# Performance work log

Measured on AMD Instinct MI355X. Metric: run time of the kernel, lower is better.

Reference implementation:

```python
import jax, jax.numpy as jnp
import numpy as np

N_NODES = 50000
N_EDGES = 800000
N_GRAPHS = 256
IN_DIM = 128
HID = 64
HEADS = 4
N_CLASSES = 2
NEG_SLOPE = 0.2


def gat_conv(h, W, attn_l, attn_r, bias, src, dst, n_heads, out_dim):
    """DGL-style GATConv. h: [N, Fin] -> [N, H, D]."""
    n = h.shape[0]
    feat = (h @ W).reshape(n, n_heads, out_dim)            # [N,H,D]
    el = jnp.sum(feat * attn_l, axis=-1)                   # [N,H]
    er = jnp.sum(feat * attn_r, axis=-1)                   # [N,H]
    e = jax.nn.leaky_relu(el[src] + er[dst], NEG_SLOPE)    # [E,H]
    # edge softmax over incoming edges of each dst node (numerically stable)
    emax = jax.ops.segment_max(e, dst, num_segments=n)     # [N,H]
    emax = jnp.where(jnp.isfinite(emax), emax, 0.0)
    ee = jnp.exp(e - emax[dst])                            # [E,H]
    denom = jax.ops.segment_sum(ee, dst, num_segments=n)   # [N,H]
    alpha = ee / jnp.maximum(denom, 1e-9)[dst]             # [E,H]
    msg = alpha[:, :, None] * feat[src]                    # [E,H,D]
    rst = jax.ops.segment_sum(msg, dst, num_segments=n)    # [N,H,D]
    return rst + bias.reshape(1, n_heads, out_dim)


def setup_inputs() -> dict:
    key = jax.random.key(0)
    ks = jax.random.split(key, 16)
    h = jax.random.normal(ks[0], (N_NODES, IN_DIM), dtype=jnp.float32)
    src = jax.random.randint(ks[1], (N_EDGES,), 0, N_NODES, dtype=jnp.int32)
    dst = jax.random.randint(ks[2], (N_EDGES,), 0, N_NODES, dtype=jnp.int32)
    graph_ids = jnp.sort(jax.random.randint(ks[3], (N_NODES,), 0, N_GRAPHS, dtype=jnp.int32))
    s1 = 1.0 / np.sqrt(IN_DIM)
    s2 = 1.0 / np.sqrt(HID * HEADS)
    sc = 1.0 / np.sqrt(HID)
    W1 = jax.random.normal(ks[4], (IN_DIM, HEADS * HID), dtype=jnp.float32) * s1
    attn_l1 = jax.random.normal(ks[5], (HEADS, HID), dtype=jnp.float32) * sc
    attn_r1 = jax.random.normal(ks[6], (HEADS, HID), dtype=jnp.float32) * sc
    b1 = jnp.zeros((HEADS * HID,), dtype=jnp.float32)
    W2 = jax.random.normal(ks[7], (HEADS * HID, 1 * HID), dtype=jnp.float32) * s2
    attn_l2 = jax.random.normal(ks[8], (1, HID), dtype=jnp.float32) * sc
    attn_r2 = jax.random.normal(ks[9], (1, HID), dtype=jnp.float32) * sc
    b2 = jnp.zeros((HID,), dtype=jnp.float32)
    Wc = jax.random.normal(ks[10], (HID, N_CLASSES), dtype=jnp.float32) * sc
    bc = jnp.zeros((N_CLASSES,), dtype=jnp.float32)
    return {"h": h, "src": src, "dst": dst, "graph_ids": graph_ids,
            "W1": W1, "attn_l1": attn_l1, "attn_r1": attn_r1, "b1": b1,
            "W2": W2, "attn_l2": attn_l2, "attn_r2": attn_r2, "b2": b2,
            "Wc": Wc, "bc": bc}


def reference(h, src, dst, graph_ids, W1, attn_l1, attn_r1, b1,
              W2, attn_l2, attn_r2, b2, Wc, bc):
    # layer 1: [N, IN] -> [N, HEADS, HID] -> relu -> flatten heads
    x = jax.nn.relu(gat_conv(h, W1, attn_l1, attn_r1, b1, src, dst, HEADS, HID))
    x = x.reshape(N_NODES, HEADS * HID)
    # layer 2: single head -> [N, HID]
    x = jax.nn.relu(gat_conv(x, W2, attn_l2, attn_r2, b2, src, dst, 1, HID))
    x = x.reshape(N_NODES, HID)
    # dropout p=0.3 is identity at eval time
    # AvgPooling: mean of node features per graph
    sums = jax.ops.segment_sum(x, graph_ids, num_segments=N_GRAPHS)      # [G,HID]
    cnts = jax.ops.segment_sum(jnp.ones((N_NODES,), x.dtype), graph_ids,
                               num_segments=N_GRAPHS)                    # [G]
    pooled = sums / jnp.maximum(cnts, 1.0)[:, None]
    return pooled @ Wc + bc                                              # [G, n_classes]
```

## Files before the change

kernel.cpp:

```cpp
#include <hip/hip_runtime.h>
#include <math.h>

#define NN 50000
#define NE 800000
#define NG 256
#define IND 128
#define NBUCK 98
#define CHUNK 4096
#define NPBLK ((NE + CHUNK - 1) / CHUNK)

typedef __bf16 bf16_t;
typedef bf16_t bf16x8 __attribute__((ext_vector_type(8)));
typedef float f32x4 __attribute__((ext_vector_type(4)));
typedef float floatx2 __attribute__((ext_vector_type(2)));
typedef unsigned short ushortx8 __attribute__((ext_vector_type(8)));

__device__ __forceinline__ float lrelu(float x) { return fmaxf(x, 0.2f * x); }
__device__ __forceinline__ float b2f(unsigned short u) {
  return __uint_as_float(((unsigned)u) << 16);
}
__device__ __forceinline__ unsigned short f2b(float f) {
  unsigned u = __float_as_uint(f);
  return (unsigned short)((u + 0x7fffu + ((u >> 16) & 1u)) >> 16);
}
__device__ __forceinline__ float sel4(float v0, float v1, float v2, float v3, int g) {
  float a01 = (g & 1) ? v1 : v0;
  float a23 = (g & 1) ? v3 : v2;
  return (g & 2) ? a23 : a01;
}

__global__ __launch_bounds__(256) void k_prep(const float* __restrict__ W1,
                                              const int* __restrict__ dst,
                                              unsigned short* __restrict__ w1t_hi,
                                              int* __restrict__ counts) {
  int tid = blockIdx.x * 256 + threadIdx.x;
  if (tid < 256 * IND) {
    int c = tid >> 7, k = tid & 127;
    w1t_hi[tid] = f2b(W1[(size_t)k * 256 + c]);
  }
  if (tid < NE) atomicAdd(&counts[dst[tid]], 1);
}

__global__ __launch_bounds__(256) void k_gemm1(const float* __restrict__ h,
                                               const unsigned short* __restrict__ w1t_hi,
                                               const float* __restrict__ al,
                                               const float* __restrict__ ar,
                                               unsigned int* __restrict__ feat1f8,
                                               float4* __restrict__ el1,
                                               float4* __restrict__ er1) {
  __shared__ unsigned short w1s[256 * IND];
  int t = threadIdx.x;
  for (int i = t; i < 4096; i += 256) {
    int c = i >> 4, k8 = i & 15;
    ushortx8 v = ((const ushortx8*)w1t_hi)[i];
    int byte = (c * 256 + k8 * 16) ^ ((c & 7) << 4);
    *(ushortx8*)((char*)w1s + byte) = v;
  }
  __syncthreads();
  int w = t >> 6, l = t & 63;
  int c0 = l & 15, kg = l >> 4;
  int rw = blockIdx.x * 64 + w * 16;
  int arow = rw + c0;
  if (arow >= NN) arow = NN - 1;
  const float4* hp = (const float4*)h + (size_t)arow * 32 + kg * 2;
  f32x4 acc[16] = {};
#pragma unroll
  for (int ks = 0; ks < 4; ks++) {
    float4 v0 = hp[ks * 8], v1 = hp[ks * 8 + 1];
    float f[8] = {v0.x, v0.y, v0.z, v0.w, v1.x, v1.y, v1.z, v1.w};
    ushortx8 uh, ul;
#pragma unroll
    for (int j = 0; j < 8; j++) {
      unsigned short hj = f2b(f[j]);
      uh[j] = hj;
      ul[j] = f2b(f[j] - b2f(hj));
    }
    bf16x8 ah = *(bf16x8*)&uh;
    bf16x8 alo = *(bf16x8*)&ul;
#pragma unroll
    for (int n = 0; n < 16; n++) {
      int col = n * 16 + c0;
      int byte = (col * 256 + (ks * 4 + kg) * 16) ^ ((col & 7) << 4);
      bf16x8 b = *(const bf16x8*)(const void*)((const char*)w1s + byte);
      acc[n] = __builtin_amdgcn_mfma_f32_16x16x32_bf16(alo, b, acc[n], 0, 0, 0);
      acc[n] = __builtin_amdgcn_mfma_f32_16x16x32_bf16(ah, b, acc[n], 0, 0, 0);
    }
  }
  float alv[16], arv[16];
#pragma unroll
  for (int n = 0; n < 16; n++) {
    int ai = (n >> 2) * 64 + (n & 3) * 16 + c0;
    alv[n] = al[ai];
    arv[n] = ar[ai];
  }
#pragma unroll
  for (int j = 0; j < 4; j++) {
    int node = rw + kg * 4 + j;
    bool ok = node < NN;
    float pl[4] = {0.f, 0.f, 0.f, 0.f}, pr[4] = {0.f, 0.f, 0.f, 0.f};
#pragma unroll
    for (int dq = 0; dq < 4; dq++) {
      float v0 = acc[dq][j], v1 = acc[4 | dq][j], v2 = acc[8 | dq][j], v3 = acc[12 | dq][j];
      if (ok) {
        int u = __builtin_amdgcn_cvt_pk_fp8_f32(v0, v1, 0, false);
        u = __builtin_amdgcn_cvt_pk_fp8_f32(v2, v3, u, true);
        feat1f8[(size_t)node * 64 + dq * 16 + c0] = (unsigned)u;
      }
    }
#pragma unroll
    for (int n = 0; n < 16; n++) {
      float cv = acc[n][j];
      int hh = n >> 2;
      pl[hh] += cv * alv[n];
      pr[hh] += cv * arv[n];
    }
#pragma unroll
    for (int off = 1; off < 16; off <<= 1) {
#pragma unroll
      for (int hh = 0; hh < 4; hh++) {
        pl[hh] += __shfl_xor(pl[hh], off);
        pr[hh] += __shfl_xor(pr[hh], off);
      }
    }
    if (c0 == 0 && ok) {
      el1[node] = make_float4(pl[0], pl[1], pl[2], pl[3]);
      er1[node] = make_float4(pr[0], pr[1], pr[2], pr[3]);
    }
  }
}

#define NSB ((NN + 1023) / 1024)
__global__ __launch_bounds__(1024) void k_scanA(const int* __restrict__ counts,
                                                int* __restrict__ bsums) {
  int gid = blockIdx.x * 1024 + threadIdx.x;
  int v = (gid < NN) ? counts[gid] : 0;
#pragma unroll
  for (int off = 32; off; off >>= 1) v += __shfl_xor(v, off);
  __shared__ int ws[16];
  int w = threadIdx.x >> 6, l = threadIdx.x & 63;
  if (l == 0) ws[w] = v;
  __syncthreads();
  if (threadIdx.x == 0) {
    int s = 0;
#pragma unroll
    for (int i = 0; i < 16; i++) s += ws[i];
    bsums[blockIdx.x] = s;
  }
}

__global__ __launch_bounds__(64) void k_scanB(const int* __restrict__ bsums,
                                              int* __restrict__ boffs,
                                              int* __restrict__ bcursor) {
  int l = threadIdx.x;
  int orig = (l < NSB) ? bsums[l] : 0;
  int v = orig;
#pragma unroll
  for (int off = 1; off < 64; off <<= 1) {
    int tv = __shfl_up(v, off);
    if (l >= off) v += tv;
  }
  if (l < NSB) boffs[l] = v - orig;
  for (int i = l; i < NBUCK; i += 64) bcursor[i] = 0;
}

__global__ __launch_bounds__(1024) void k_scanC(const int* __restrict__ counts,
                                                const int* __restrict__ boffs,
                                                int* __restrict__ offs) {
  int gid = blockIdx.x * 1024 + threadIdx.x;
  int orig = (gid < NN) ? counts[gid] : 0;
  int v = orig;
  int w = threadIdx.x >> 6, l = threadIdx.x & 63;
#pragma unroll
  for (int off = 1; off < 64; off <<= 1) {
    int tv = __shfl_up(v, off);
    if (l >= off) v += tv;
  }
  __shared__ int ws[16];
  if (l == 63) ws[w] = v;
  __syncthreads();
  int woff = 0;
#pragma unroll
  for (int i = 0; i < 16; i++)
    if (i < w) woff += ws[i];
  if (gid < NN) offs[gid] = boffs[blockIdx.x] + woff + v - orig;
  if (gid == 0) offs[NN] = NE;
}

__global__ __launch_bounds__(256) void k_part(const int* __restrict__ src, const int* __restrict__ dst,
                                              const int* __restrict__ offs, int* __restrict__ bcursor,
                                              int2* __restrict__ ebuf) {
  __shared__ int lcnt[NBUCK];
  __shared__ int lbase[NBUCK];
  __shared__ int gb[NBUCK];
  int t = threadIdx.x;
  for (int i = t; i < NBUCK; i += 256) lcnt[i] = 0;
  __syncthreads();
  int e0 = blockIdx.x * CHUNK;
  int sv[16], dv[16], rk[16];
#pragma unroll
  for (int i = 0; i < 16; i++) {
    int e = e0 + i * 256 + t;
    if (e < NE) {
      sv[i] = src[e];
      dv[i] = dst[e];
      rk[i] = atomicAdd(&lcnt[dv[i] >> 9], 1);
    }
  }
  __syncthreads();
  for (int i = t; i < NBUCK; i += 256) {
    lbase[i] = atomicAdd(&bcursor[i], lcnt[i]);
    gb[i] = offs[i << 9];
  }
  __syncthreads();
#pragma unroll
  for (int i = 0; i < 16; i++) {
    int e = e0 + i * 256 + t;
    if (e < NE) {
      int b = dv[i] >> 9;
      int2 v;
      v.x = sv[i];
      v.y = dv[i];
      ebuf[gb[b] + lbase[b] + rk[i]] = v;
    }
  }
}

__global__ __launch_bounds__(256) void k_scat2(const int2* __restrict__ ebuf, const int* __restrict__ offs,
                                               int2* __restrict__ sd) {
  __shared__ int lcur[512];
  int b = blockIdx.x, t = threadIdx.x;
  for (int i = t; i < 512; i += 256) lcur[i] = 0;
  int n0 = b << 9;
  int n1 = n0 + 512;
  if (n1 > NN) n1 = NN;
  int lo = offs[n0], hi = offs[n1];
  __syncthreads();
  for (int i = lo + t; i < hi; i += 256) {
    int2 p = ebuf[i];
    int pos = atomicAdd(&lcur[p.y - n0], 1);
    sd[offs[p.y] + pos] = p;
  }
}

__global__ __launch_bounds__(256) void k_edge1(const int2* __restrict__ sd,
                                               const float4* __restrict__ el1,
                                               const float4* __restrict__ er1,
                                               ushort4* __restrict__ ee1) {
  int i = blockIdx.x * 256 + threadIdx.x;
  if (i >= NE) return;
  int2 p = sd[i];
  float4 l = el1[p.x], r = er1[p.y];
  ushort4 o;
  o.x = f2b(__expf(lrelu(l.x + r.x)));
  o.y = f2b(__expf(lrelu(l.y + r.y)));
  o.z = f2b(__expf(lrelu(l.z + r.z)));
  o.w = f2b(__expf(lrelu(l.w + r.w)));
  ee1[i] = o;
}

__global__ __launch_bounds__(256) void k_agg1(const int* __restrict__ offs, const int2* __restrict__ sd,
                                              const ushort4* __restrict__ ee1,
                                              const unsigned int* __restrict__ feat1f8,
                                              const float* __restrict__ b1,
                                              unsigned short* __restrict__ x1b) {
  int wid = (blockIdx.x * 256 + threadIdx.x) >> 6;
  int lane = threadIdx.x & 63;
  if (wid >= NN) return;
  int g = lane >> 4, q = lane & 15;
  int start = offs[wid], end = offs[wid + 1];
  float a[4][4] = {};
  float ds0 = 0.f, ds1 = 0.f, ds2 = 0.f, ds3 = 0.f;
  for (int i = start; i < end; i += 4) {
    int e = i + g;
    bool valid = e < end;
    int ec = valid ? e : end - 1;
    int s = sd[ec].x;
    ushort4 wq = ee1[ec];
    float4 wv;
    wv.x = b2f(wq.x); wv.y = b2f(wq.y); wv.z = b2f(wq.z); wv.w = b2f(wq.w);
    if (!valid) { wv.x = 0.f; wv.y = 0.f; wv.z = 0.f; wv.w = 0.f; }
    uint4 u = *(const uint4*)(feat1f8 + (size_t)s * 64 + q * 4);
#pragma unroll
    for (int dj = 0; dj < 4; dj++) {
      unsigned uu = (&u.x)[dj];
      floatx2 lo = __builtin_amdgcn_cvt_pk_f32_fp8(uu, false);
      floatx2 hi = __builtin_amdgcn_cvt_pk_f32_fp8(uu, true);
      a[dj][0] += wv.x * lo[0];
      a[dj][1] += wv.y * lo[1];
      a[dj][2] += wv.z * hi[0];
      a[dj][3] += wv.w * hi[1];
    }
    ds0 += wv.x; ds1 += wv.y; ds2 += wv.z; ds3 += wv.w;
  }
#pragma unroll
  for (int off = 16; off < 64; off <<= 1) {
#pragma unroll
    for (int dj = 0; dj < 4; dj++) {
#pragma unroll
      for (int hh = 0; hh < 4; hh++) a[dj][hh] += __shfl_xor(a[dj][hh], off);
    }
    ds0 += __shfl_xor(ds0, off);
    ds1 += __shfl_xor(ds1, off);
    ds2 += __shfl_xor(ds2, off);
    ds3 += __shfl_xor(ds3, off);
  }
  float dsg = sel4(ds0, ds1, ds2, ds3, g);
  float inv = 1.f / fmaxf(dsg, 1e-9f);
  float4 bb = *(const float4*)(b1 + g * 64 + q * 4);
  ushort4 ov;
  ov.x = f2b(fmaxf(sel4(a[0][0], a[0][1], a[0][2], a[0][3], g) * inv + bb.x, 0.f));
  ov.y = f2b(fmaxf(sel4(a[1][0], a[1][1], a[1][2], a[1][3], g) * inv + bb.y, 0.f));
  ov.z = f2b(fmaxf(sel4(a[2][0], a[2][1], a[2][2], a[2][3], g) * inv + bb.z, 0.f));
  ov.w = f2b(fmaxf(sel4(a[3][0], a[3][1], a[3][2], a[3][3], g) * inv + bb.w, 0.f));
  *(ushort4*)(x1b + (size_t)wid * 256 + g * 64 + q * 4) = ov;
}

__global__ __launch_bounds__(256) void k_gemm2(const unsigned short* __restrict__ x1b,
                                               const float* __restrict__ W2,
                                               const float* __restrict__ al2,
                                               const float* __restrict__ ar2,
                                               unsigned int* __restrict__ feat2f8,
                                               float* __restrict__ el2,
                                               float* __restrict__ er2) {
  __shared__ unsigned short w2t[64 * 256];
  int t = threadIdx.x;
  for (int i = t; i < 64 * 256; i += 256) {
    int k = i >> 6, col = i & 63;
    int kg = k >> 3;
    int s = (col * 32 + kg) ^ (col & 7);
    w2t[s * 8 + (k & 7)] = f2b(W2[i]);
  }
  __syncthreads();
  int w = t >> 6, l = t & 63;
  int rw = blockIdx.x * 64 + w * 16;
  int arow = rw + (l & 15);
  if (arow >= NN) arow = NN - 1;
  const unsigned short* aptr = x1b + (size_t)arow * 256 + (l >> 4) * 8;
  f32x4 acc[4] = {};
#pragma unroll
  for (int ks = 0; ks < 8; ks++) {
    bf16x8 a = *(const bf16x8*)(const void*)(aptr + ks * 32);
#pragma unroll
    for (int n = 0; n < 4; n++) {
      int colg = n * 16 + (l & 15);
      int kg = ks * 4 + (l >> 4);
      int s = (colg * 32 + kg) ^ (colg & 7);
      bf16x8 b = *(const bf16x8*)(const void*)&w2t[s * 8];
      acc[n] = __builtin_amdgcn_mfma_f32_16x16x32_bf16(a, b, acc[n], 0, 0, 0);
    }
  }
  float al2v[4], ar2v[4];
#pragma unroll
  for (int n = 0; n < 4; n++) { al2v[n] = al2[n * 16 + (l & 15)]; ar2v[n] = ar2[n * 16 + (l & 15)]; }
#pragma unroll
  for (int j = 0; j < 4; j++) {
    int node = rw + (l >> 4) * 4 + j;
    float pl = 0.f, pr = 0.f;
    float c0v = acc[0][j], c1v = acc[1][j], c2v = acc[2][j], c3v = acc[3][j];
    if (node < NN) {
      int u = __builtin_amdgcn_cvt_pk_fp8_f32(c0v, c1v, 0, false);
      u = __builtin_amdgcn_cvt_pk_fp8_f32(c2v, c3v, u, true);
      feat2f8[(size_t)node * 16 + (l & 15)] = (unsigned)u;
    }
    pl = c0v * al2v[0] + c1v * al2v[1] + c2v * al2v[2] + c3v * al2v[3];
    pr = c0v * ar2v[0] + c1v * ar2v[1] + c2v * ar2v[2] + c3v * ar2v[3];
#pragma unroll
    for (int off = 1; off < 16; off <<= 1) {
      pl += __shfl_xor(pl, off);
      pr += __shfl_xor(pr, off);
    }
    if ((l & 15) == 0 && node < NN) { el2[node] = pl; er2[node] = pr; }
  }
}

__global__ __launch_bounds__(256) void k_edge2(const int2* __restrict__ sd,
                                               const float* __restrict__ el2,
                                               const float* __restrict__ er2,
                                               float* __restrict__ ee2) {
  int i = blockIdx.x * 256 + threadIdx.x;
  if (i >= NE) return;
  int2 p = sd[i];
  ee2[i] = __expf(lrelu(el2[p.x] + er2[p.y]));
}

__global__ __launch_bounds__(256) void k_agg2(const int* __restrict__ offs, const int2* __restrict__ sd,
                                              const float* __restrict__ ee2,
                                              const unsigned int* __restrict__ feat2f8,
                                              const float* __restrict__ b2, const int* __restrict__ gid,
                                              float* __restrict__ psum) {
  int wid = (blockIdx.x * 256 + threadIdx.x) >> 6;
  int lane = threadIdx.x & 63;
  if (wid >= NN) return;
  int g = lane >> 4, q = lane & 15;
  int start = offs[wid], end = offs[wid + 1];
  float a0 = 0.f, a1 = 0.f, a2 = 0.f, a3 = 0.f, dsum = 0.f;
  for (int i = start; i < end; i += 4) {
    int e = i + g;
    bool valid = e < end;
    int ec = valid ? e : end - 1;
    int s = sd[ec].x;
    float wv = valid ? ee2[ec] : 0.f;
    unsigned u = feat2f8[(size_t)s * 16 + q];
    floatx2 lo = __builtin_amdgcn_cvt_pk_f32_fp8(u, false);
    floatx2 hi = __builtin_amdgcn_cvt_pk_f32_fp8(u, true);
    a0 += wv * lo[0];
    a1 += wv * lo[1];
    a2 += wv * hi[0];
    a3 += wv * hi[1];
    dsum += wv;
  }
#pragma unroll
  for (int off = 16; off < 64; off <<= 1) {
    a0 += __shfl_xor(a0, off);
    a1 += __shfl_xor(a1, off);
    a2 += __shfl_xor(a2, off);
    a3 += __shfl_xor(a3, off);
    dsum += __shfl_xor(dsum, off);
  }
  float inv = 1.f / fmaxf(dsum, 1e-9f);
  float av = sel4(a0, a1, a2, a3, g);
  float v = fmaxf(av * inv + b2[lane], 0.f);
  atomicAdd(&psum[gid[wid] * 64 + lane], v);
}

__global__ __launch_bounds__(256) void k_head(const float* __restrict__ psum, const int* __restrict__ gid,
                                              const float* __restrict__ Wc, const float* __restrict__ bc,
                                              float* __restrict__ out) {
  int wid = (blockIdx.x * 256 + threadIdx.x) >> 6;
  int lane = threadIdx.x & 63;
  if (wid >= NG) return;
  int g = wid;
  int lo = 0, hi = NN;
  while (lo < hi) { int mid = (lo + hi) >> 1; if (gid[mid] < g) lo = mid + 1; else hi = mid; }
  int lb = lo;
  hi = NN;
  while (lo < hi) { int mid = (lo + hi) >> 1; if (gid[mid] < g + 1) lo = mid + 1; else hi = mid; }
  int cnt = lo - lb;
  float inv = 1.f / fmaxf((float)cnt, 1.f);
  float p = psum[g * 64 + lane] * inv;
  float a0 = p * Wc[lane * 2 + 0];
  float a1 = p * Wc[lane * 2 + 1];
#pragma unroll
  for (int off = 32; off; off >>= 1) { a0 += __shfl_xor(a0, off); a1 += __shfl_xor(a1, off); }
  if (lane == 0) { out[g * 2 + 0] = a0 + bc[0]; out[g * 2 + 1] = a1 + bc[1]; }
}

extern "C" void kernel_launch(void* const* d_in, const int* in_sizes, int n_in,
                              void* d_out, int out_size, void* d_ws, size_t ws_size,
                              hipStream_t stream) {
  const float* h = (const float*)d_in[0];
  const int* src = (const int*)d_in[1];
  const int* dst = (const int*)d_in[2];
  const int* gid = (const int*)d_in[3];
  const float* W1 = (const float*)d_in[4];
  const float* al1 = (const float*)d_in[5];
  const float* ar1 = (const float*)d_in[6];
  const float* b1 = (const float*)d_in[7];
  const float* W2 = (const float*)d_in[8];
  const float* al2 = (const float*)d_in[9];
  const float* ar2 = (const float*)d_in[10];
  const float* b2 = (const float*)d_in[11];
  const float* Wc = (const float*)d_in[12];
  const float* bc = (const float*)d_in[13];
  float* out = (float*)d_out;

  char* wsp = (char*)d_ws;
  size_t off = 0;
  auto take = [&](size_t bytes) -> void* {
    void* p = wsp + off;
    off = (off + bytes + 255) & ~(size_t)255;
    return p;
  };
  unsigned int* feat1f8 = (unsigned int*)take((size_t)NN * 256);
  unsigned short* x1b = (unsigned short*)take((size_t)NN * 256 * 2);
  unsigned int* feat2f8 = (unsigned int*)take((size_t)NN * 64);
  unsigned short* w1t_hi = (unsigned short*)take((size_t)256 * IND * 2);
  float4* el1 = (float4*)take((size_t)NN * 16);
  float4* er1 = (float4*)take((size_t)NN * 16);
  float* el2 = (float*)take((size_t)NN * 4);
  float* er2 = (float*)take((size_t)NN * 4);
  int* counts = (int*)take((size_t)NN * 4);
  int* offs = (int*)take((size_t)(NN + 1) * 4);
  int2* sd = (int2*)take((size_t)NE * 8);
  int2* ebuf = (int2*)take((size_t)NE * 8);
  ushort4* ee1 = (ushort4*)take((size_t)NE * 8);
  float* ee2 = (float*)take((size_t)NE * 4);
  float* psum = (float*)take((size_t)NG * 64 * 4);
  int* bsums = (int*)take((size_t)NSB * 4);
  int* boffs = (int*)take((size_t)NSB * 4);
  int* bcursor = (int*)take((size_t)NBUCK * 4);

  hipMemsetAsync(counts, 0, (size_t)NN * 4, stream);
  hipMemsetAsync(psum, 0, (size_t)NG * 64 * 4, stream);

  k_prep<<<(NE + 255) / 256, 256, 0, stream>>>(W1, dst, w1t_hi, counts);

  k_scanA<<<NSB, 1024, 0, stream>>>(counts, bsums);
  k_scanB<<<1, 64, 0, stream>>>(bsums, boffs, bcursor);
  k_scanC<<<NSB, 1024, 0, stream>>>(counts, boffs, offs);
  k_part<<<NPBLK, 256, 0, stream>>>(src, dst, offs, bcursor, ebuf);
  k_scat2<<<NBUCK, 256, 0, stream>>>(ebuf, offs, sd);

  k_gemm1<<<(NN + 63) / 64, 256, 0, stream>>>(h, w1t_hi, al1, ar1, feat1f8, el1, er1);
  k_edge1<<<(NE + 255) / 256, 256, 0, stream>>>(sd, el1, er1, ee1);
  k_agg1<<<(NN * 64 + 255) / 256, 256, 0, stream>>>(offs, sd, ee1, feat1f8, b1, x1b);

  k_gemm2<<<(NN + 63) / 64, 256, 0, stream>>>(x1b, W2, al2, ar2, feat2f8, el2, er2);
  k_edge2<<<(NE + 255) / 256, 256, 0, stream>>>(sd, el2, er2, ee2);
  k_agg2<<<(NN * 64 + 255) / 256, 256, 0, stream>>>(offs, sd, ee2, feat2f8, b2, gid, psum);

  k_head<<<(NG * 64 + 255) / 256, 256, 0, stream>>>(psum, gid, Wc, bc, out);
}
```

Before: 226.8 us.

## Replace atomic graph pooling with bf16 node buffer and per-graph reduction kernel

Layer-2 aggregation now writes per-node outputs as bf16 to a workspace buffer instead of atomically adding into per-graph sums. A new pooling kernel, one 1024-thread block per graph, binary-searches the graph's node range, sums rows in 16 slices through shared memory, then applies the classifier. This removes heavy atomic contention (3.2M atomics onto 16K addresses) and the psum memset, at the cost of an extra 6.4MB write/read round trip and bf16 rounding of layer-2 outputs.

```diff
diff --git a/kernel.cpp b/kernel.cpp
--- a/kernel.cpp
+++ b/kernel.cpp
@@ -386,8 +386,8 @@
 __global__ __launch_bounds__(256) void k_agg2(const int* __restrict__ offs, const int2* __restrict__ sd,
                                               const float* __restrict__ ee2,
                                               const unsigned int* __restrict__ feat2f8,
-                                              const float* __restrict__ b2, const int* __restrict__ gid,
-                                              float* __restrict__ psum) {
+                                              const float* __restrict__ b2,
+                                              unsigned short* __restrict__ x2b) {
   int wid = (blockIdx.x * 256 + threadIdx.x) >> 6;
   int lane = threadIdx.x & 63;
   if (wid >= NN) return;
@@ -419,30 +419,39 @@
   }
   float inv = 1.f / fmaxf(dsum, 1e-9f);
   float av = sel4(a0, a1, a2, a3, g);
-  float v = fmaxf(av * inv + b2[lane], 0.f);
-  atomicAdd(&psum[gid[wid] * 64 + lane], v);
-}
-
-__global__ __launch_bounds__(256) void k_head(const float* __restrict__ psum, const int* __restrict__ gid,
-                                              const float* __restrict__ Wc, const float* __restrict__ bc,
-                                              float* __restrict__ out) {
-  int wid = (blockIdx.x * 256 + threadIdx.x) >> 6;
-  int lane = threadIdx.x & 63;
-  if (wid >= NG) return;
-  int g = wid;
+  x2b[(size_t)wid * 64 + lane] = f2b(fmaxf(av * inv + b2[lane], 0.f));
+}
+
+__global__ __launch_bounds__(1024) void k_pool(const unsigned short* __restrict__ x2b,
+                                               const int* __restrict__ gid,
+                                               const float* __restrict__ Wc,
+                                               const float* __restrict__ bc,
+                                               float* __restrict__ out) {
+  int g = blockIdx.x;
+  int t = threadIdx.x;
   int lo = 0, hi = NN;
   while (lo < hi) { int mid = (lo + hi) >> 1; if (gid[mid] < g) lo = mid + 1; else hi = mid; }
   int lb = lo;
   hi = NN;
   while (lo < hi) { int mid = (lo + hi) >> 1; if (gid[mid] < g + 1) lo = mid + 1; else hi = mid; }
-  int cnt = lo - lb;
-  float inv = 1.f / fmaxf((float)cnt, 1.f);
-  float p = psum[g * 64 + lane] * inv;
-  float a0 = p * Wc[lane * 2 + 0];
-  float a1 = p * Wc[lane * 2 + 1];
-#pragma unroll
-  for (int off = 32; off; off >>= 1) { a0 += __shfl_xor(a0, off); a1 += __shfl_xor(a1, off); }
-  if (lane == 0) { out[g * 2 + 0] = a0 + bc[0]; out[g * 2 + 1] = a1 + bc[1]; }
+  int le = lo;
+  int d = t & 63, slice = t >> 6;
+  float s = 0.f;
+  for (int n = lb + slice; n < le; n += 16) s += b2f(x2b[(size_t)n * 64 + d]);
+  __shared__ float ws[16][64];
+  ws[slice][d] = s;
+  __syncthreads();
+  if (t < 64) {
+    float p = 0.f;
+#pragma unroll
+    for (int i = 0; i < 16; i++) p += ws[i][d];
+    p /= fmaxf((float)(le - lb), 1.f);
+    float a0 = p * Wc[d * 2 + 0];
+    float a1 = p * Wc[d * 2 + 1];
+#pragma unroll
+    for (int off = 32; off; off >>= 1) { a0 += __shfl_xor(a0, off); a1 += __shfl_xor(a1, off); }
+    if (d == 0) { out[g * 2 + 0] = a0 + bc[0]; out[g * 2 + 1] = a1 + bc[1]; }
+  }
 }
 
 extern "C" void kernel_launch(void* const* d_in, const int* in_sizes, int n_in,
@@ -474,6 +483,7 @@
   unsigned int* feat1f8 = (unsigned int*)take((size_t)NN * 256);
   unsigned short* x1b = (unsigned short*)take((size_t)NN * 256 * 2);
   unsigned int* feat2f8 = (unsigned int*)take((size_t)NN * 64);
+  unsigned short* x2b = (unsigned short*)take((size_t)NN * 64 * 2);
   unsigned short* w1t_hi = (unsigned short*)take((size_t)256 * IND * 2);
   float4* el1 = (float4*)take((size_t)NN * 16);
   float4* er1 = (float4*)take((size_t)NN * 16);
@@ -485,13 +495,11 @@
   int2* ebuf = (int2*)take((size_t)NE * 8);
   ushort4* ee1 = (ushort4*)take((size_t)NE * 8);
   float* ee2 = (float*)take((size_t)NE * 4);
-  float* psum = (float*)take((size_t)NG * 64 * 4);
   int* bsums = (int*)take((size_t)NSB * 4);
   int* boffs = (int*)take((size_t)NSB * 4);
   int* bcursor = (int*)take((size_t)NBUCK * 4);
 
   hipMemsetAsync(counts, 0, (size_t)NN * 4, stream);
-  hipMemsetAsync(psum, 0, (size_t)NG * 64 * 4, stream);
 
   k_prep<<<(NE + 255) / 256, 256, 0, stream>>>(W1, dst, w1t_hi, counts);
 
@@ -507,7 +515,7 @@
 
   k_gemm2<<<(NN + 63) / 64, 256, 0, stream>>>(x1b, W2, al2, ar2, feat2f8, el2, er2);
   k_edge2<<<(NE + 255) / 256, 256, 0, stream>>>(sd, el2, er2, ee2);
-  k_agg2<<<(NN * 64 + 255) / 256, 256, 0, stream>>>(offs, sd, ee2, feat2f8, b2, gid, psum);
-
-  k_head<<<(NG * 64 + 255) / 256, 256, 0, stream>>>(psum, gid, Wc, bc, out);
-}
+  k_agg2<<<(NN * 64 + 255) / 256, 256, 0, stream>>>(offs, sd, ee2, feat2f8, b2, x2b);
+
+  k_pool<<<NG, 1024, 0, stream>>>(x2b, gid, Wc, bc, out);
+}
```

Result: faster. 212.7 us (-6.2%).
